# Kernel tuning notes

Measured on AMD Instinct MI355X. Metric: run time of the kernel, lower is better.

Reference implementation:

```python
import jax, jax.numpy as jnp
import numpy as np

D = 256
H = 4
HD = D // H


def setup_inputs() -> dict:
    key = jax.random.key(0)
    ks = jax.random.split(key, 12)
    A, T = 64, 512
    s = 1.0 / np.sqrt(D)
    return {
        "features": jax.random.normal(ks[0], (A, T, D), jnp.float32),
        "positions": jax.random.normal(ks[1], (A, T, 2), jnp.float32),
        "Wq": jax.random.normal(ks[2], (D, D), jnp.float32) * s,
        "bq": jnp.zeros((D,), jnp.float32),
        "Wk": jax.random.normal(ks[3], (D, D), jnp.float32) * s,
        "bk": jnp.zeros((D,), jnp.float32),
        "Wv": jax.random.normal(ks[4], (D, D), jnp.float32) * s,
        "bv": jnp.zeros((D,), jnp.float32),
        "Wo": jax.random.normal(ks[5], (D, D), jnp.float32) * s,
        "bo": jnp.zeros((D,), jnp.float32),
        "max_distance": 2,
        "time_window": 64,
    }


def _sparse_mask(positions, max_distance, time_window):
    # positions: [A, T, 2] -> allowed [A, T, T]
    A, T, _ = positions.shape
    diff = positions[:, :, None, :] - positions[:, None, :, :]  # [A,T,T,2]
    dist2 = jnp.sum(diff * diff, axis=-1)                       # [A,T,T]
    t = jnp.arange(T)
    tmask = jnp.abs(t[:, None] - t[None, :]) <= time_window      # [T,T]
    return (dist2 <= float(max_distance) ** 2) & tmask[None]     # [A,T,T]


def reference(features, positions, Wq, bq, Wk, bk, Wv, bv, Wo, bo,
              max_distance, time_window):
    A, T, Dm = features.shape
    allowed = _sparse_mask(positions, max_distance, time_window)  # [A,T,T]
    q = features @ Wq.T + bq
    k = features @ Wk.T + bk
    v = features @ Wv.T + bv
    # split heads: [A, T, H, HD]
    q = q.reshape(A, T, H, HD)
    k = k.reshape(A, T, H, HD)
    v = v.reshape(A, T, H, HD)
    scale = 1.0 / np.sqrt(HD)
    scores = jnp.einsum("athd,ashd->ahts", q, k) * scale          # [A,H,T,T]
    scores = jnp.where(allowed[:, None], scores, -jnp.inf)
    attn = jax.nn.softmax(scores, axis=-1)
    out = jnp.einsum("ahts,ashd->athd", attn, v).reshape(A, T, Dm)
    return out @ Wo.T + bo
```

## Files before the change

### kernel.cpp

```cpp
#include <hip/hip_runtime.h>
#include <hip/hip_bf16.h>
#include <cstdint>
#include <cstddef>

typedef __attribute__((ext_vector_type(8))) _Float16 half8;
typedef __attribute__((ext_vector_type(4))) float floatx4;

#define MFMA16(a, b, c) __builtin_amdgcn_mfma_f32_16x16x32_f16((a), (b), (c), 0, 0, 0)

#define GLOAD_LDS16(g, l)                                                     \
    __builtin_amdgcn_global_load_lds(                                         \
        (const __attribute__((address_space(1))) void*)(g),                   \
        (__attribute__((address_space(3))) void*)(l), 16, 0, 0)

#define NFEAT 8388608


__device__ __forceinline__ void stage_dma(
    const _Float16* __restrict__ src, _Float16* __restrict__ lds,
    int wid, int lane)
{
#pragma unroll
    for (int i = 0; i < 4; ++i) {
        int grp = wid * 4 + i;
        int row = grp * 8 + (lane >> 3);
        int sc  = (lane & 7) ^ (row & 7);
        GLOAD_LDS16(src + (size_t)row * 256 + sc * 8, lds + grp * 512);
    }
}

__device__ __forceinline__ void stage_f32(
    const float* __restrict__ src, _Float16* __restrict__ lds, int tid)
{
#pragma unroll
    for (int i = 0; i < 4; ++i) {
        int g   = tid + 256 * i;
        int row = g >> 3, chd = g & 7;
        int chs = chd ^ (row & 7);
        const float* s = src + (size_t)row * 256 + chs * 8;
        float4 v0 = *(const float4*)s;
        float4 v1 = *(const float4*)(s + 4);
        half8 h = { (_Float16)v0.x, (_Float16)v0.y, (_Float16)v0.z, (_Float16)v0.w,
                    (_Float16)v1.x, (_Float16)v1.y, (_Float16)v1.z, (_Float16)v1.w };
        *(half8*)(&lds[row * 64 + chd * 8]) = h;
    }
}

template <bool XF32, bool OUT_HALF>
__device__ __forceinline__ void gemm128x128(
    const void* __restrict__ Xv, const float* __restrict__ Wf,
    const float* __restrict__ bias, void* __restrict__ Cptr, int bm, int bn)
{
    __shared__ _Float16 As[128 * 64];
    __shared__ _Float16 Bs[128 * 64];

    const int tid  = threadIdx.x;
    const int lane = tid & 63, wid = tid >> 6;
    const int quad = lane >> 4, l16 = lane & 15;
    const int wm = wid & 1, wn = wid >> 1;

    floatx4 acc[4][4] = {};
    const float* Wg = Wf + (size_t)bn * 128 * 256;

    for (int k0 = 0; k0 < 256; k0 += 64) {
        if (XF32)
            stage_f32(((const float*)Xv) + (size_t)bm * 128 * 256 + k0, As, tid);
        else
            stage_dma(((const _Float16*)Xv) + (size_t)bm * 128 * 256 + k0, As, wid, lane);
        stage_f32(Wg + k0, Bs, tid);
        __syncthreads();
#pragma unroll
        for (int kh = 0; kh < 2; ++kh) {
            half8 af[4], bf[4];
#pragma unroll
            for (int mi = 0; mi < 4; ++mi) {
                int row = wm * 64 + mi * 16 + l16;
                int ch  = (kh * 4 + quad) ^ (l16 & 7);
                af[mi] = *(const half8*)(&As[row * 64 + ch * 8]);
            }
#pragma unroll
            for (int ni = 0; ni < 4; ++ni) {
                int row = wn * 64 + ni * 16 + l16;
                int ch  = (kh * 4 + quad) ^ (l16 & 7);
                bf[ni] = *(const half8*)(&Bs[row * 64 + ch * 8]);
            }
#pragma unroll
            for (int mi = 0; mi < 4; ++mi)
#pragma unroll
                for (int ni = 0; ni < 4; ++ni)
                    acc[mi][ni] = MFMA16(af[mi], bf[ni], acc[mi][ni]);
        }
        __syncthreads();
    }

#pragma unroll
    for (int ni = 0; ni < 4; ++ni) {
        int col = bn * 128 + wn * 64 + ni * 16 + l16;
        float bv = bias[col];
#pragma unroll
        for (int mi = 0; mi < 4; ++mi) {
#pragma unroll
            for (int r = 0; r < 4; ++r) {
                int row = bm * 128 + wm * 64 + mi * 16 + quad * 4 + r;
                float v = acc[mi][ni][r] + bv;
                if (OUT_HALF)
                    ((_Float16*)Cptr)[(size_t)row * 256 + col] = (_Float16)v;
                else
                    ((float*)Cptr)[(size_t)row * 256 + col] = v;
            }
        }
    }
}

__global__ __launch_bounds__(256) void qkv_gemm(
    const float* __restrict__ feat,
    const float* __restrict__ Wq, const float* __restrict__ Wk,
    const float* __restrict__ Wv,
    const float* __restrict__ bq, const float* __restrict__ bk,
    const float* __restrict__ bv,
    _Float16* __restrict__ Qb, _Float16* __restrict__ Kb, _Float16* __restrict__ Vb)
{
    int z = blockIdx.x >> 1, bn = blockIdx.x & 1;
    const float* W    = (z == 0) ? Wq : (z == 1) ? Wk : Wv;
    const float* bias = (z == 0) ? bq : (z == 1) ? bk : bv;
    _Float16* out     = (z == 0) ? Qb : (z == 1) ? Kb : Vb;
    gemm128x128<true, true>(feat, W, bias, out, blockIdx.y, bn);
}

__global__ __launch_bounds__(256) void out_gemm(
    const _Float16* __restrict__ attnH, const float* __restrict__ Wo,
    const float* __restrict__ bo, float* __restrict__ out)
{
    gemm128x128<false, false>(attnH, Wo, bo, out, blockIdx.y, blockIdx.x);
}

__global__ __launch_bounds__(256) void attn_kernel(
    const _Float16* __restrict__ Qb, const _Float16* __restrict__ Kb,
    const _Float16* __restrict__ Vb, const float* __restrict__ positions,
    const int* __restrict__ mdp, const int* __restrict__ twp,
    _Float16* __restrict__ attnb)
{
    const int qt = blockIdx.x, h = blockIdx.y, a = blockIdx.z;
    const int q0 = qt * 64;
    const int s_base = q0 - 64;
    const int tid = threadIdx.x, lane = tid & 63, wid = tid >> 6;
    const int quad = lane >> 4, l16 = lane & 15;

    __shared__ _Float16 KPs[192 * 64];
    __shared__ _Float16 Vt[64 * 196];

    const size_t abase = (size_t)a * 512;
    const int md = *mdp, tw = *twp;
    const float md2 = (float)(md * md);

    const size_t qrow = abase + q0 + wid * 16 + l16;
    half8 aq0 = *(const half8*)(Qb + qrow * 256 + h * 64 + quad * 8);
    half8 aq1 = *(const half8*)(Qb + qrow * 256 + h * 64 + 32 + quad * 8);
    float qpx[4], qpy[4];
    int trow[4];
#pragma unroll
    for (int r = 0; r < 4; ++r) {
        int m = wid * 16 + quad * 4 + r;
        trow[r] = q0 + m;
        float2 qp = *(const float2*)(positions + (abase + q0 + m) * 2);
        qpx[r] = qp.x;
        qpy[r] = qp.y;
    }

#pragma unroll
    for (int i = 0; i < 6; ++i) {
        int grp = wid * 6 + i;
        int si  = grp * 8 + (lane >> 3);
        int sc  = min(max(s_base + si, 0), 511);
        int ch  = (lane & 7) ^ (si & 7);
        GLOAD_LDS16(Kb + (abase + sc) * 256 + h * 64 + ch * 8, KPs + grp * 512);
    }
#pragma unroll
    for (int i = 0; i < 3; ++i) {
        int idx = tid + 256 * i;
        int si2 = (idx % 96) * 2;
        int d0  = (idx / 96) * 8;
        int sa  = min(max(s_base + si2, 0), 511);
        int sb  = min(max(s_base + si2 + 1, 0), 511);
        half8 v0 = *(const half8*)(Vb + (abase + sa) * 256 + h * 64 + d0);
        half8 v1 = *(const half8*)(Vb + (abase + sb) * 256 + h * 64 + d0);
#pragma unroll
        for (int j = 0; j < 8; ++j) {
            union { _Float16 hh[2]; uint32_t u; } p;
            p.hh[0] = v0[j]; p.hh[1] = v1[j];
            *(uint32_t*)(&Vt[(d0 + j) * 196 + si2]) = p.u;
        }
    }
    __syncthreads();

    floatx4 S[12];
#pragma unroll
    for (int j = 0; j < 12; ++j) {
        int si = j * 16 + l16;
        half8 bk0 = *(const half8*)(&KPs[si * 64 + ((quad) ^ (si & 7)) * 8]);
        half8 bk1 = *(const half8*)(&KPs[si * 64 + ((4 + quad) ^ (si & 7)) * 8]);
        floatx4 acc = {};
        acc = MFMA16(aq0, bk0, acc);
        acc = MFMA16(aq1, bk1, acc);
        int sr = s_base + si;
        int sc = min(max(sr, 0), 511);
        float2 kp = *(const float2*)(positions + (abase + sc) * 2);
        bool svalid = (sr >= 0) && (sr < 512);
#pragma unroll
        for (int r = 0; r < 4; ++r) {
            float dx = qpx[r] - kp.x, dy = qpy[r] - kp.y;
            float d2 = dx * dx + dy * dy;
            int dt = trow[r] - sr; dt = dt < 0 ? -dt : dt;
            bool ok = svalid && (d2 <= md2) && (dt <= tw);
            S[j][r] = ok ? acc[r] * 0.125f : -1e30f;
        }
    }

    float minv[4];
#pragma unroll
    for (int r = 0; r < 4; ++r) {
        float m = -1e30f;
#pragma unroll
        for (int j = 0; j < 12; ++j) m = fmaxf(m, S[j][r]);
        m = fmaxf(m, __shfl_xor(m, 1));
        m = fmaxf(m, __shfl_xor(m, 2));
        m = fmaxf(m, __shfl_xor(m, 4));
        m = fmaxf(m, __shfl_xor(m, 8));
        float l = 0.f;
#pragma unroll
        for (int j = 0; j < 12; ++j) {
            float p = __expf(S[j][r] - m);
            S[j][r] = p;
            l += p;
        }
        l += __shfl_xor(l, 1);
        l += __shfl_xor(l, 2);
        l += __shfl_xor(l, 4);
        l += __shfl_xor(l, 8);
        minv[r] = 1.0f / l;
    }

    __syncthreads();

    _Float16* Ps = KPs + wid * (16 * 192);
#pragma unroll
    for (int j = 0; j < 12; ++j)
#pragma unroll
        for (int r = 0; r < 4; ++r) {
            int row = quad * 4 + r;
            int col = j * 16 + l16;
            int ch  = (col >> 3) ^ (row & 7);
            Ps[row * 192 + ch * 8 + (col & 7)] = (_Float16)(S[j][r] * minv[r]);
        }

    half8 af[6];
#pragma unroll
    for (int k = 0; k < 6; ++k) {
        int ch = (k * 4 + quad) ^ (l16 & 7);
        af[k] = *(const half8*)(&Ps[l16 * 192 + ch * 8]);
    }
#pragma unroll
    for (int n = 0; n < 4; ++n) {
        floatx4 accO = {};
#pragma unroll
        for (int k = 0; k < 6; ++k) {
            half8 bv = *(const half8*)(&Vt[(n * 16 + l16) * 196 + k * 32 + quad * 8]);
            accO = MFMA16(af[k], bv, accO);
        }
#pragma unroll
        for (int r = 0; r < 4; ++r) {
            int row = q0 + wid * 16 + quad * 4 + r;
            attnb[(abase + row) * 256 + h * 64 + n * 16 + l16] = (_Float16)accO[r];
        }
    }
}

extern "C" void kernel_launch(void* const* d_in, const int* in_sizes, int n_in,
                              void* d_out, int out_size, void* d_ws, size_t ws_size,
                              hipStream_t stream)
{
    const float* feat = (const float*)d_in[0];
    const float* pos  = (const float*)d_in[1];
    const float* Wq   = (const float*)d_in[2];
    const float* bq   = (const float*)d_in[3];
    const float* Wk   = (const float*)d_in[4];
    const float* bk   = (const float*)d_in[5];
    const float* Wv   = (const float*)d_in[6];
    const float* bv   = (const float*)d_in[7];
    const float* Wo   = (const float*)d_in[8];
    const float* bo   = (const float*)d_in[9];
    const int*   md   = (const int*)d_in[10];
    const int*   tw   = (const int*)d_in[11];
    float*       out  = (float*)d_out;

    _Float16* ws    = (_Float16*)d_ws;
    _Float16* Qb    = ws;
    _Float16* Kb    = Qb + NFEAT;
    _Float16* Vb    = Kb + NFEAT;
    _Float16* attnH = Vb + NFEAT;

    dim3 gqkv(6, 256);
    qkv_gemm<<<gqkv, 256, 0, stream>>>(feat, Wq, Wk, Wv, bq, bk, bv, Qb, Kb, Vb);

    dim3 gattn(8, 4, 64);
    attn_kernel<<<gattn, 256, 0, stream>>>(Qb, Kb, Vb, pos, md, tw, attnH);

    dim3 gout(2, 256);
    out_gemm<<<gout, 256, 0, stream>>>(attnH, Wo, bo, out);
}
```

Measured before the change: 193.5 us.

## Reuse staged features across Q/K/V, remap blocks for XCD locality, swizzle V tile

The QKV projection now stages a full 128x256 feature tile into LDS once, converting from fp32 only once, and loops over the three weight matrices instead of launching separate blocks per matrix. All three kernels use a 1D grid whose block index is remapped so neighbouring tiles land on the same XCD, which should improve L2 reuse. The transposed V tile in the attention kernel drops the padded stride in favour of an XOR swizzle to avoid LDS bank conflicts. In exchange the QKV kernel uses more LDS and has fewer, longer blocks, which may lower occupancy.

```diff
diff --git a/kernel.cpp b/kernel.cpp
--- a/kernel.cpp
+++ b/kernel.cpp
@@ -14,7 +14,6 @@
         (__attribute__((address_space(3))) void*)(l), 16, 0, 0)
 
 #define NFEAT 8388608
-
 
 __device__ __forceinline__ void stage_dma(
     const _Float16* __restrict__ src, _Float16* __restrict__ lds,
@@ -29,8 +28,9 @@
     }
 }
 
-__device__ __forceinline__ void stage_f32(
-    const float* __restrict__ src, _Float16* __restrict__ lds, int tid)
+__device__ __forceinline__ void stage_f32_s(
+    const float* __restrict__ src, _Float16* __restrict__ lds, int tid,
+    int dst_stride)
 {
 #pragma unroll
     for (int i = 0; i < 4; ++i) {
@@ -42,77 +42,11 @@
         float4 v1 = *(const float4*)(s + 4);
         half8 h = { (_Float16)v0.x, (_Float16)v0.y, (_Float16)v0.z, (_Float16)v0.w,
                     (_Float16)v1.x, (_Float16)v1.y, (_Float16)v1.z, (_Float16)v1.w };
-        *(half8*)(&lds[row * 64 + chd * 8]) = h;
-    }
-}
-
-template <bool XF32, bool OUT_HALF>
-__device__ __forceinline__ void gemm128x128(
-    const void* __restrict__ Xv, const float* __restrict__ Wf,
-    const float* __restrict__ bias, void* __restrict__ Cptr, int bm, int bn)
-{
-    __shared__ _Float16 As[128 * 64];
-    __shared__ _Float16 Bs[128 * 64];
-
-    const int tid  = threadIdx.x;
-    const int lane = tid & 63, wid = tid >> 6;
-    const int quad = lane >> 4, l16 = lane & 15;
-    const int wm = wid & 1, wn = wid >> 1;
-
-    floatx4 acc[4][4] = {};
-    const float* Wg = Wf + (size_t)bn * 128 * 256;
-
-    for (int k0 = 0; k0 < 256; k0 += 64) {
-        if (XF32)
-            stage_f32(((const float*)Xv) + (size_t)bm * 128 * 256 + k0, As, tid);
-        else
-            stage_dma(((const _Float16*)Xv) + (size_t)bm * 128 * 256 + k0, As, wid, lane);
-        stage_f32(Wg + k0, Bs, tid);
-        __syncthreads();
-#pragma unroll
-        for (int kh = 0; kh < 2; ++kh) {
-            half8 af[4], bf[4];
-#pragma unroll
-            for (int mi = 0; mi < 4; ++mi) {
-                int row = wm * 64 + mi * 16 + l16;
-                int ch  = (kh * 4 + quad) ^ (l16 & 7);
-                af[mi] = *(const half8*)(&As[row * 64 + ch * 8]);
-            }
-#pragma unroll
-            for (int ni = 0; ni < 4; ++ni) {
-                int row = wn * 64 + ni * 16 + l16;
-                int ch  = (kh * 4 + quad) ^ (l16 & 7);
-                bf[ni] = *(const half8*)(&Bs[row * 64 + ch * 8]);
-            }
-#pragma unroll
-            for (int mi = 0; mi < 4; ++mi)
-#pragma unroll
-                for (int ni = 0; ni < 4; ++ni)
-                    acc[mi][ni] = MFMA16(af[mi], bf[ni], acc[mi][ni]);
-        }
-        __syncthreads();
-    }
-
-#pragma unroll
-    for (int ni = 0; ni < 4; ++ni) {
-        int col = bn * 128 + wn * 64 + ni * 16 + l16;
-        float bv = bias[col];
-#pragma unroll
-        for (int mi = 0; mi < 4; ++mi) {
-#pragma unroll
-            for (int r = 0; r < 4; ++r) {
-                int row = bm * 128 + wm * 64 + mi * 16 + quad * 4 + r;
-                float v = acc[mi][ni][r] + bv;
-                if (OUT_HALF)
-                    ((_Float16*)Cptr)[(size_t)row * 256 + col] = (_Float16)v;
-                else
-                    ((float*)Cptr)[(size_t)row * 256 + col] = v;
-            }
-        }
-    }
-}
-
-__global__ __launch_bounds__(256) void qkv_gemm(
+        *(half8*)(&lds[row * dst_stride + chd * 8]) = h;
+    }
+}
+
+__global__ __launch_bounds__(256) void qkv_fused(
     const float* __restrict__ feat,
     const float* __restrict__ Wq, const float* __restrict__ Wk,
     const float* __restrict__ Wv,
@@ -120,18 +54,136 @@
     const float* __restrict__ bv,
     _Float16* __restrict__ Qb, _Float16* __restrict__ Kb, _Float16* __restrict__ Vb)
 {
-    int z = blockIdx.x >> 1, bn = blockIdx.x & 1;
-    const float* W    = (z == 0) ? Wq : (z == 1) ? Wk : Wv;
-    const float* bias = (z == 0) ? bq : (z == 1) ? bk : bv;
-    _Float16* out     = (z == 0) ? Qb : (z == 1) ? Kb : Vb;
-    gemm128x128<true, true>(feat, W, bias, out, blockIdx.y, bn);
+    __shared__ _Float16 Xs[128 * 256];
+    __shared__ _Float16 Ws[128 * 64];
+
+    const int n   = blockIdx.x;
+    const int idx = n >> 3;
+    const int bm  = (n & 7) * 32 + (idx >> 1);
+    const int bn  = idx & 1;
+
+    const int tid  = threadIdx.x;
+    const int lane = tid & 63, wid = tid >> 6;
+    const int quad = lane >> 4, l16 = lane & 15;
+    const int wm = wid & 1, wn = wid >> 1;
+
+    const float* Xg = feat + (size_t)bm * 128 * 256;
+#pragma unroll
+    for (int slab = 0; slab < 4; ++slab)
+        stage_f32_s(Xg + slab * 64, Xs + slab * 64, tid, 256);
+    __syncthreads();
+
+#pragma unroll 1
+    for (int z = 0; z < 3; ++z) {
+        const float* W    = (z == 0) ? Wq : (z == 1) ? Wk : Wv;
+        const float* bias = (z == 0) ? bq : (z == 1) ? bk : bv;
+        _Float16*    outp = (z == 0) ? Qb : (z == 1) ? Kb : Vb;
+        const float* Wg = W + (size_t)bn * 128 * 256;
+
+        floatx4 acc[4][4] = {};
+#pragma unroll 1
+        for (int ks = 0; ks < 4; ++ks) {
+            stage_f32_s(Wg + ks * 64, Ws, tid, 64);
+            __syncthreads();
+#pragma unroll
+            for (int kh = 0; kh < 2; ++kh) {
+                half8 af[4], bf[4];
+#pragma unroll
+                for (int mi = 0; mi < 4; ++mi) {
+                    int row = wm * 64 + mi * 16 + l16;
+                    int cs  = (kh * 4 + quad) ^ (row & 7);
+                    af[mi] = *(const half8*)(&Xs[row * 256 + ks * 64 + cs * 8]);
+                }
+#pragma unroll
+                for (int ni = 0; ni < 4; ++ni) {
+                    int row = wn * 64 + ni * 16 + l16;
+                    int cs  = (kh * 4 + quad) ^ (row & 7);
+                    bf[ni] = *(const half8*)(&Ws[row * 64 + cs * 8]);
+                }
+#pragma unroll
+                for (int mi = 0; mi < 4; ++mi)
+#pragma unroll
+                    for (int ni = 0; ni < 4; ++ni)
+                        acc[mi][ni] = MFMA16(af[mi], bf[ni], acc[mi][ni]);
+            }
+            __syncthreads();
+        }
+
+#pragma unroll
+        for (int ni = 0; ni < 4; ++ni) {
+            int col = bn * 128 + wn * 64 + ni * 16 + l16;
+            float bv2 = bias[col];
+#pragma unroll
+            for (int mi = 0; mi < 4; ++mi)
+#pragma unroll
+                for (int r = 0; r < 4; ++r) {
+                    int row = bm * 128 + wm * 64 + mi * 16 + quad * 4 + r;
+                    outp[(size_t)row * 256 + col] = (_Float16)(acc[mi][ni][r] + bv2);
+                }
+        }
+    }
 }
 
 __global__ __launch_bounds__(256) void out_gemm(
     const _Float16* __restrict__ attnH, const float* __restrict__ Wo,
     const float* __restrict__ bo, float* __restrict__ out)
 {
-    gemm128x128<false, false>(attnH, Wo, bo, out, blockIdx.y, blockIdx.x);
+    __shared__ _Float16 As[128 * 64];
+    __shared__ _Float16 Bs[128 * 64];
+
+    const int n   = blockIdx.x;
+    const int idx = n >> 3;
+    const int bm  = (n & 7) * 32 + (idx >> 1);
+    const int bn  = idx & 1;
+
+    const int tid  = threadIdx.x;
+    const int lane = tid & 63, wid = tid >> 6;
+    const int quad = lane >> 4, l16 = lane & 15;
+    const int wm = wid & 1, wn = wid >> 1;
+
+    floatx4 acc[4][4] = {};
+    const float* Wg = Wo + (size_t)bn * 128 * 256;
+
+    for (int k0 = 0; k0 < 256; k0 += 64) {
+        stage_dma(attnH + (size_t)bm * 128 * 256 + k0, As, wid, lane);
+        stage_f32_s(Wg + k0, Bs, tid, 64);
+        __syncthreads();
+#pragma unroll
+        for (int kh = 0; kh < 2; ++kh) {
+            half8 af[4], bf[4];
+#pragma unroll
+            for (int mi = 0; mi < 4; ++mi) {
+                int row = wm * 64 + mi * 16 + l16;
+                int cs  = (kh * 4 + quad) ^ (row & 7);
+                af[mi] = *(const half8*)(&As[row * 64 + cs * 8]);
+            }
+#pragma unroll
+            for (int ni = 0; ni < 4; ++ni) {
+                int row = wn * 64 + ni * 16 + l16;
+                int cs  = (kh * 4 + quad) ^ (row & 7);
+                bf[ni] = *(const half8*)(&Bs[row * 64 + cs * 8]);
+            }
+#pragma unroll
+            for (int mi = 0; mi < 4; ++mi)
+#pragma unroll
+                for (int ni = 0; ni < 4; ++ni)
+                    acc[mi][ni] = MFMA16(af[mi], bf[ni], acc[mi][ni]);
+        }
+        __syncthreads();
+    }
+
+#pragma unroll
+    for (int ni = 0; ni < 4; ++ni) {
+        int col = bn * 128 + wn * 64 + ni * 16 + l16;
+        float bv = bo[col];
+#pragma unroll
+        for (int mi = 0; mi < 4; ++mi)
+#pragma unroll
+            for (int r = 0; r < 4; ++r) {
+                int row = bm * 128 + wm * 64 + mi * 16 + quad * 4 + r;
+                out[(size_t)row * 256 + col] = acc[mi][ni][r] + bv;
+            }
+    }
 }
 
 __global__ __launch_bounds__(256) void attn_kernel(
@@ -140,14 +192,19 @@
     const int* __restrict__ mdp, const int* __restrict__ twp,
     _Float16* __restrict__ attnb)
 {
-    const int qt = blockIdx.x, h = blockIdx.y, a = blockIdx.z;
+    const int n   = blockIdx.x;
+    const int idx = n >> 3;
+    const int a   = (n & 7) * 8 + (idx >> 5);
+    const int rem = idx & 31;
+    const int qt  = rem >> 2, h = rem & 3;
+
     const int q0 = qt * 64;
     const int s_base = q0 - 64;
     const int tid = threadIdx.x, lane = tid & 63, wid = tid >> 6;
     const int quad = lane >> 4, l16 = lane & 15;
 
     __shared__ _Float16 KPs[192 * 64];
-    __shared__ _Float16 Vt[64 * 196];
+    __shared__ _Float16 Vt[64 * 192];
 
     const size_t abase = (size_t)a * 512;
     const int md = *mdp, tw = *twp;
@@ -177,18 +234,21 @@
     }
 #pragma unroll
     for (int i = 0; i < 3; ++i) {
-        int idx = tid + 256 * i;
-        int si2 = (idx % 96) * 2;
-        int d0  = (idx / 96) * 8;
+        int g   = tid + 256 * i;
+        int si2 = (g % 96) * 2;
+        int d0  = (g / 96) * 8;
         int sa  = min(max(s_base + si2, 0), 511);
         int sb  = min(max(s_base + si2 + 1, 0), 511);
         half8 v0 = *(const half8*)(Vb + (abase + sa) * 256 + h * 64 + d0);
         half8 v1 = *(const half8*)(Vb + (abase + sb) * 256 + h * 64 + d0);
+        int c = si2 >> 3;
 #pragma unroll
         for (int j = 0; j < 8; ++j) {
+            int d  = d0 + j;
+            int cs = (c & ~7) | ((c & 7) ^ (d & 7));
             union { _Float16 hh[2]; uint32_t u; } p;
             p.hh[0] = v0[j]; p.hh[1] = v1[j];
-            *(uint32_t*)(&Vt[(d0 + j) * 196 + si2]) = p.u;
+            *(uint32_t*)(&Vt[d * 192 + cs * 8 + (si2 & 7)]) = p.u;
         }
     }
     __syncthreads();
@@ -260,17 +320,20 @@
         af[k] = *(const half8*)(&Ps[l16 * 192 + ch * 8]);
     }
 #pragma unroll
-    for (int n = 0; n < 4; ++n) {
+    for (int nn = 0; nn < 4; ++nn) {
         floatx4 accO = {};
 #pragma unroll
         for (int k = 0; k < 6; ++k) {
-            half8 bv = *(const half8*)(&Vt[(n * 16 + l16) * 196 + k * 32 + quad * 8]);
+            int row = nn * 16 + l16;
+            int c   = k * 4 + quad;
+            int cs  = (c & ~7) | ((c & 7) ^ (row & 7));
+            half8 bv = *(const half8*)(&Vt[row * 192 + cs * 8]);
             accO = MFMA16(af[k], bv, accO);
         }
 #pragma unroll
         for (int r = 0; r < 4; ++r) {
             int row = q0 + wid * 16 + quad * 4 + r;
-            attnb[(abase + row) * 256 + h * 64 + n * 16 + l16] = (_Float16)accO[r];
+            attnb[(abase + row) * 256 + h * 64 + nn * 16 + l16] = (_Float16)accO[r];
         }
     }
 }
@@ -299,12 +362,9 @@
     _Float16* Vb    = Kb + NFEAT;
     _Float16* attnH = Vb + NFEAT;
 
-    dim3 gqkv(6, 256);
-    qkv_gemm<<<gqkv, 256, 0, stream>>>(feat, Wq, Wk, Wv, bq, bk, bv, Qb, Kb, Vb);
-
-    dim3 gattn(8, 4, 64);
-    attn_kernel<<<gattn, 256, 0, stream>>>(Qb, Kb, Vb, pos, md, tw, attnH);
-
-    dim3 gout(2, 256);
-    out_gemm<<<gout, 256, 0, stream>>>(attnH, Wo, bo, out);
-}
+    qkv_fused<<<512, 256, 0, stream>>>(feat, Wq, Wk, Wv, bq, bk, bv, Qb, Kb, Vb);
+
+    attn_kernel<<<2048, 256, 0, stream>>>(Qb, Kb, Vb, pos, md, tw, attnH);
+
+    out_gemm<<<512, 256, 0, stream>>>(attnH, Wo, bo, out);
+}
```

New measurement: 167.7 us. -13.4%, faster.
